# Kernel optimization log

Hardware: AMD Instinct MI355X
Metric: run time of the kernel (lower is better)

Reference implementation:

```python
import jax, jax.numpy as jnp
import numpy as np
from jax import lax

B, S, D = 4, 128, 256
POOL = 3


def conv_block(x, w, b, stride, pool_k):
    # x: (N, Cin, H, W), w: (Cout, Cin, kh, kw)
    y = lax.conv_general_dilated(
        x, w, window_strides=(stride, stride), padding='VALID',
        dimension_numbers=('NCHW', 'OIHW', 'NCHW'))
    y = y + b[None, :, None, None]
    y = jax.nn.gelu(y, approximate=False)  # torch GELU default is exact
    # MaxPool2d(kernel_size=pool_k) -> stride = pool_k, VALID
    y = lax.reduce_window(y, -jnp.inf, lax.max,
                          (1, 1, pool_k, pool_k), (1, 1, pool_k, pool_k), 'VALID')
    return y


def setup_inputs() -> dict:
    key = jax.random.key(0)
    ks = jax.random.split(key, 8)
    token_features = jax.random.normal(ks[0], (B, S, D), dtype=jnp.float32)
    type_embedds = jax.random.normal(ks[1], (B, S, D), dtype=jnp.float32)
    # Conv2dFeatures(depth=3, num_channels=16, start_kernel=3, start_stride=2, pool_kernel=3)
    w1 = jax.random.normal(ks[2], (16, 1, 3, 3), dtype=jnp.float32) * 0.1
    b1 = jax.random.normal(ks[3], (16,), dtype=jnp.float32) * 0.01
    w2 = jax.random.normal(ks[4], (32, 16, 3, 3), dtype=jnp.float32) * 0.05
    b2 = jax.random.normal(ks[5], (32,), dtype=jnp.float32) * 0.01
    w3 = jax.random.normal(ks[6], (32, 32, 3, 3), dtype=jnp.float32) * 0.05
    b3 = jax.random.normal(ks[7], (32,), dtype=jnp.float32) * 0.01
    return dict(token_features=token_features, type_embedds=type_embedds,
                w1=w1, b1=b1, w2=w2, b2=b2, w3=w3, b3=b3)


def reference(token_features, type_embedds, w1, b1, w2, b2, w3, b3):
    b, s, d = type_embedds.shape
    # Outter2dFusion: fused[n,s,i,j] = type_embedds[n,s,i] * token_features[n,s,j]
    fused = jnp.einsum('bsi,bsj->bsij', type_embedds, token_features)
    # Conv stack applied per seq position with in_channels=1 == one batched conv
    x = fused.reshape(b * s, 1, d, d)
    x = conv_block(x, w1, b1, stride=2, pool_k=POOL)
    x = conv_block(x, w2, b2, stride=1, pool_k=POOL)
    x = conv_block(x, w3, b3, stride=1, pool_k=POOL)
    # Dropout is identity in eval mode
    return x.reshape(b, s, -1)
```

## Files before the change

kernel.cpp:

```cpp
#include <hip/hip_runtime.h>
#include <math.h>


#define NIMG 512

__device__ __forceinline__ float gelu_exact(float x) {
    return 0.5f * x * (1.0f + erff(x * 0.70710678118654752f));
}
__device__ __forceinline__ float pool_gelu(float vmin, float vmax) {
    return fmaxf(gelu_exact(vmin), gelu_exact(vmax));
}

typedef __attribute__((address_space(3))) char lds_char;
typedef const __attribute__((address_space(1))) char glb_char;
__device__ __forceinline__ void gl_lds16(const void* g, void* l) {
    __builtin_amdgcn_global_load_lds((glb_char*)g, (lds_char*)l, 16, 0, 0);
}

__global__ __launch_bounds__(256) void k1_fused(const float* __restrict__ tok,
                                                const float* __restrict__ typ,
                                                const float* __restrict__ w1,
                                                const float* __restrict__ b1,
                                                float* __restrict__ s1) {
    const int blk = blockIdx.x;
    const int img = blk >> 1;
    const int py0 = (blk & 1) * 21;
    const int tid = threadIdx.x;
    const int c     = tid >> 4;
    const int pslot = tid & 15;

    float wv[9];
#pragma unroll
    for (int k = 0; k < 9; ++k) wv[k] = w1[c * 9 + k];
    const float bias = b1[c];

    const float* frow = tok + img * 256;
    const float* trow = typ + img * 256;

    float g[3][3][3];
    int pxv[3];
#pragma unroll
    for (int s = 0; s < 3; ++s) {
        const int px = pslot + 16 * s;
        pxv[s] = px;
        const int pe = px < 42 ? px : 41;
        float f7[7];
#pragma unroll
        for (int q = 0; q < 7; ++q) f7[q] = frow[6 * pe + q];
#pragma unroll
        for (int di = 0; di < 3; ++di)
#pragma unroll
            for (int wx = 0; wx < 3; ++wx)
                g[s][di][wx] = wv[di * 3 + 0] * f7[2 * wx]
                             + wv[di * 3 + 1] * f7[2 * wx + 1]
                             + wv[di * 3 + 2] * f7[2 * wx + 2];
    }

    float* orow = s1 + ((size_t)img * 16 + c) * (42 * 44);
    for (int py = py0; py < py0 + 21; ++py) {
        float ts[7];
#pragma unroll
        for (int q = 0; q < 7; ++q) ts[q] = trow[6 * py + q];
#pragma unroll
        for (int s = 0; s < 3; ++s) {
            float vmin = INFINITY, vmax = -INFINITY;
#pragma unroll
            for (int wy = 0; wy < 3; ++wy) {
#pragma unroll
                for (int wx = 0; wx < 3; ++wx) {
                    float v = ts[2 * wy] * g[s][0][wx];
                    v = fmaf(ts[2 * wy + 1], g[s][1][wx], v);
                    v = fmaf(ts[2 * wy + 2], g[s][2][wx], v);
                    vmin = fminf(vmin, v);
                    vmax = fmaxf(vmax, v);
                }
            }
            if (pxv[s] < 42)
                orow[py * 44 + pxv[s]] = pool_gelu(vmin + bias, vmax + bias);
        }
    }
}

__global__ __launch_bounds__(256) void k2_conv(const float* __restrict__ s1,
                                               const float* __restrict__ w2,
                                               const float* __restrict__ b2,
                                               float* __restrict__ s2) {
    const int blk = blockIdx.x;
    const int img = blk >> 1;
    const int cog = blk & 1;
    __shared__ float4 slab4[3][512];

    const int tid  = threadIdx.x;
    const int lane = tid & 63;
    const int grp  = tid >> 6;
    const int wbase64 = tid & ~63;

    int base[3], valid[3], py[3], px[3];
#pragma unroll
    for (int tI = 0; tI < 3; ++tI) {
        const int cc0 = lane + 64 * tI;
        valid[tI] = (cc0 < 169);
        const int cc = valid[tI] ? cc0 : 168;
        py[tI] = cc / 13;
        px[tI] = cc % 13;
        base[tI] = py[tI] * 132 + px[tI] * 3;
    }

    float acc[4][3][9];
#pragma unroll
    for (int a = 0; a < 4; ++a)
#pragma unroll
        for (int tI = 0; tI < 3; ++tI)
#pragma unroll
            for (int k = 0; k < 9; ++k) acc[a][tI][k] = 0.f;

    const float* s1img = s1 + (size_t)img * 16 * 1848;

#pragma unroll
    for (int p = 0; p < 2; ++p) {
        const char* src = (const char*)(s1img + p * 1848);
        gl_lds16(src + (size_t)tid * 16,         (char*)&slab4[p][0] + (size_t)wbase64 * 16);
        gl_lds16(src + (size_t)(256 + tid) * 16, (char*)&slab4[p][256] + (size_t)wbase64 * 16);
    }

#pragma unroll 1
    for (int cin = 0; cin < 16; ++cin) {
        const int cur = cin % 3;
        if (cin != 15) asm volatile("s_waitcnt vmcnt(2)" ::: "memory");
        else           asm volatile("s_waitcnt vmcnt(0)" ::: "memory");
        __builtin_amdgcn_s_barrier();

        if (cin + 2 < 16) {
            const int nb = (cin + 2) % 3;
            const char* src = (const char*)(s1img + (cin + 2) * 1848);
            gl_lds16(src + (size_t)tid * 16,         (char*)&slab4[nb][0] + (size_t)wbase64 * 16);
            gl_lds16(src + (size_t)(256 + tid) * 16, (char*)&slab4[nb][256] + (size_t)wbase64 * 16);
        }

        const int wb = __builtin_amdgcn_readfirstlane((cog * 16 + grp) * 144 + cin * 9);
        float wv[4][9];
#pragma unroll
        for (int a = 0; a < 4; ++a)
#pragma unroll
            for (int k = 0; k < 9; ++k) wv[a][k] = w2[wb + a * 576 + k];

        const float* slab = (const float*)&slab4[cur][0];
#pragma unroll
        for (int tI = 0; tI < 3; ++tI) {
            float win[5][5];
#pragma unroll
            for (int r = 0; r < 5; ++r)
#pragma unroll
                for (int c2 = 0; c2 < 5; ++c2)
                    win[r][c2] = slab[base[tI] + r * 44 + c2];
#pragma unroll
            for (int wy = 0; wy < 3; ++wy)
#pragma unroll
                for (int wx = 0; wx < 3; ++wx)
#pragma unroll
                    for (int dy = 0; dy < 3; ++dy)
#pragma unroll
                        for (int dx = 0; dx < 3; ++dx) {
                            const float v = win[wy + dy][wx + dx];
#pragma unroll
                            for (int a = 0; a < 4; ++a)
                                acc[a][tI][wy * 3 + wx] =
                                    fmaf(v, wv[a][dy * 3 + dx], acc[a][tI][wy * 3 + wx]);
                        }
        }
    }

#pragma unroll
    for (int tI = 0; tI < 3; ++tI) {
        if (valid[tI]) {
#pragma unroll
            for (int a = 0; a < 4; ++a) {
                float vmin = INFINITY, vmax = -INFINITY;
#pragma unroll
                for (int k = 0; k < 9; ++k) {
                    vmin = fminf(vmin, acc[a][tI][k]);
                    vmax = fmaxf(vmax, acc[a][tI][k]);
                }
                const int co = cog * 16 + grp + 4 * a;
                const float b = b2[co];
                s2[((img * 32 + co) * 13 + py[tI]) * 13 + px[tI]] =
                    pool_gelu(vmin + b, vmax + b);
            }
        }
    }
}

__global__ __launch_bounds__(192) void k3_conv(const float* __restrict__ s2,
                                               const float* __restrict__ w3,
                                               const float* __restrict__ b3,
                                               float* __restrict__ out) {
    const int img = blockIdx.x;
    __shared__ float wl[32 * 32 * 9];

    const int tid = threadIdx.x;
    for (int i = tid; i < 9216; i += 192) wl[i] = w3[i];
    __syncthreads();

    if (tid < 144) {
        const int cp   = tid / 9;
        const int cell = tid % 9;
        const int cy = cell / 3, cx = cell % 3;
        const int base = (3 * cy) * 13 + 3 * cx;
        const int co0 = 2 * cp, co1 = 2 * cp + 1;
        const float* s2img = s2 + (size_t)img * 5408 + base;

        float acc[2][9];
#pragma unroll
        for (int a = 0; a < 2; ++a)
#pragma unroll
            for (int k = 0; k < 9; ++k) acc[a][k] = 0.f;

#pragma unroll 1
        for (int cin = 0; cin < 32; ++cin) {
            const float* sl = s2img + cin * 169;
            float win[5][5];
#pragma unroll
            for (int r = 0; r < 5; ++r)
#pragma unroll
                for (int c2 = 0; c2 < 5; ++c2)
                    win[r][c2] = sl[r * 13 + c2];
            float wk[2][9];
#pragma unroll
            for (int k = 0; k < 9; ++k) {
                wk[0][k] = wl[(co0 * 32 + cin) * 9 + k];
                wk[1][k] = wl[(co1 * 32 + cin) * 9 + k];
            }
#pragma unroll
            for (int wy = 0; wy < 3; ++wy)
#pragma unroll
                for (int wx = 0; wx < 3; ++wx)
#pragma unroll
                    for (int dy = 0; dy < 3; ++dy)
#pragma unroll
                        for (int dx = 0; dx < 3; ++dx) {
                            const float v = win[wy + dy][wx + dx];
                            acc[0][wy * 3 + wx] = fmaf(v, wk[0][dy * 3 + dx], acc[0][wy * 3 + wx]);
                            acc[1][wy * 3 + wx] = fmaf(v, wk[1][dy * 3 + dx], acc[1][wy * 3 + wx]);
                        }
        }

#pragma unroll
        for (int a = 0; a < 2; ++a) {
            float vmin = INFINITY, vmax = -INFINITY;
#pragma unroll
            for (int k = 0; k < 9; ++k) {
                vmin = fminf(vmin, acc[a][k]);
                vmax = fmaxf(vmax, acc[a][k]);
            }
            const int co = a ? co1 : co0;
            const float b = b3[co];
            out[(size_t)img * 288 + co * 9 + cell] = pool_gelu(vmin + b, vmax + b);
        }
    }
}

extern "C" void kernel_launch(void* const* d_in, const int* in_sizes, int n_in,
                              void* d_out, int out_size, void* d_ws, size_t ws_size,
                              hipStream_t stream) {
    const float* tok = (const float*)d_in[0];
    const float* typ = (const float*)d_in[1];
    const float* w1  = (const float*)d_in[2];
    const float* b1  = (const float*)d_in[3];
    const float* w2  = (const float*)d_in[4];
    const float* b2  = (const float*)d_in[5];
    const float* w3  = (const float*)d_in[6];
    const float* b3  = (const float*)d_in[7];
    float* out = (float*)d_out;

    float* s1 = (float*)d_ws;
    float* s2 = s1 + (size_t)NIMG * 16 * 42 * 44;

    k1_fused<<<dim3(NIMG * 2), dim3(256), 0, stream>>>(tok, typ, w1, b1, s1);
    k2_conv<<<dim3(NIMG * 2), dim3(256), 0, stream>>>(s1, w2, b2, s2);
    k3_conv<<<dim3(NIMG), dim3(192), 0, stream>>>(s2, w3, b3, out);
}
```

Before: 254.7 us.

## Merge k2 channel-group blocks into one 512-thread block per image with bulk slab loads

k2 now uses one 512-thread block per image instead of two 256-thread blocks that each handled half the output channels. Each input slab is read from global memory once per image rather than twice. The three-slot per-channel LDS pipeline is replaced by two bulk phases, each loading 8 input channels (about 59KB of LDS) followed by a full wait. This gives up load/compute overlap and cuts occupancy, because LDS use grows and blocks get larger.

```diff
diff --git a/kernel.cpp b/kernel.cpp
--- a/kernel.cpp
+++ b/kernel.cpp
@@ -81,19 +81,16 @@
     }
 }
 
-__global__ __launch_bounds__(256) void k2_conv(const float* __restrict__ s1,
+__global__ __launch_bounds__(512) void k2_conv(const float* __restrict__ s1,
                                                const float* __restrict__ w2,
                                                const float* __restrict__ b2,
                                                float* __restrict__ s2) {
-    const int blk = blockIdx.x;
-    const int img = blk >> 1;
-    const int cog = blk & 1;
-    __shared__ float4 slab4[3][512];
+    const int img = blockIdx.x;
+    __shared__ float slab[8 * 1848];
 
     const int tid  = threadIdx.x;
     const int lane = tid & 63;
     const int grp  = tid >> 6;
-    const int wbase64 = tid & ~63;
 
     int base[3], valid[3], py[3], px[3];
 #pragma unroll
@@ -116,57 +113,50 @@
 
     const float* s1img = s1 + (size_t)img * 16 * 1848;
 
-#pragma unroll
+#pragma unroll 1
     for (int p = 0; p < 2; ++p) {
-        const char* src = (const char*)(s1img + p * 1848);
-        gl_lds16(src + (size_t)tid * 16,         (char*)&slab4[p][0] + (size_t)wbase64 * 16);
-        gl_lds16(src + (size_t)(256 + tid) * 16, (char*)&slab4[p][256] + (size_t)wbase64 * 16);
-    }
-
-#pragma unroll 1
-    for (int cin = 0; cin < 16; ++cin) {
-        const int cur = cin % 3;
-        if (cin != 15) asm volatile("s_waitcnt vmcnt(2)" ::: "memory");
-        else           asm volatile("s_waitcnt vmcnt(0)" ::: "memory");
-        __builtin_amdgcn_s_barrier();
-
-        if (cin + 2 < 16) {
-            const int nb = (cin + 2) % 3;
-            const char* src = (const char*)(s1img + (cin + 2) * 1848);
-            gl_lds16(src + (size_t)tid * 16,         (char*)&slab4[nb][0] + (size_t)wbase64 * 16);
-            gl_lds16(src + (size_t)(256 + tid) * 16, (char*)&slab4[nb][256] + (size_t)wbase64 * 16);
-        }
-
-        const int wb = __builtin_amdgcn_readfirstlane((cog * 16 + grp) * 144 + cin * 9);
-        float wv[4][9];
-#pragma unroll
-        for (int a = 0; a < 4; ++a)
-#pragma unroll
-            for (int k = 0; k < 9; ++k) wv[a][k] = w2[wb + a * 576 + k];
-
-        const float* slab = (const float*)&slab4[cur][0];
-#pragma unroll
-        for (int tI = 0; tI < 3; ++tI) {
-            float win[5][5];
-#pragma unroll
-            for (int r = 0; r < 5; ++r)
-#pragma unroll
-                for (int c2 = 0; c2 < 5; ++c2)
-                    win[r][c2] = slab[base[tI] + r * 44 + c2];
-#pragma unroll
-            for (int wy = 0; wy < 3; ++wy)
-#pragma unroll
-                for (int wx = 0; wx < 3; ++wx)
-#pragma unroll
-                    for (int dy = 0; dy < 3; ++dy)
-#pragma unroll
-                        for (int dx = 0; dx < 3; ++dx) {
-                            const float v = win[wy + dy][wx + dx];
-#pragma unroll
-                            for (int a = 0; a < 4; ++a)
-                                acc[a][tI][wy * 3 + wx] =
-                                    fmaf(v, wv[a][dy * 3 + dx], acc[a][tI][wy * 3 + wx]);
-                        }
+        __syncthreads();
+        const char* src = (const char*)(s1img + p * (8 * 1848));
+#pragma unroll 1
+        for (int i = tid; i < 3696; i += 512)
+            gl_lds16(src + (size_t)i * 16, (char*)slab + (size_t)(i & ~63) * 16);
+        asm volatile("s_waitcnt vmcnt(0)" ::: "memory");
+        __syncthreads();
+
+#pragma unroll 1
+        for (int c8 = 0; c8 < 8; ++c8) {
+            const int cin = p * 8 + c8;
+            const int wb = __builtin_amdgcn_readfirstlane((grp * 16 + cin) * 9);
+            float wv[4][9];
+#pragma unroll
+            for (int a = 0; a < 4; ++a)
+#pragma unroll
+                for (int k = 0; k < 9; ++k) wv[a][k] = w2[wb + a * 1152 + k];
+
+            const float* slabc = slab + c8 * 1848;
+#pragma unroll
+            for (int tI = 0; tI < 3; ++tI) {
+                float win[5][5];
+#pragma unroll
+                for (int r = 0; r < 5; ++r)
+#pragma unroll
+                    for (int c2 = 0; c2 < 5; ++c2)
+                        win[r][c2] = slabc[base[tI] + r * 44 + c2];
+#pragma unroll
+                for (int wy = 0; wy < 3; ++wy)
+#pragma unroll
+                    for (int wx = 0; wx < 3; ++wx)
+#pragma unroll
+                        for (int dy = 0; dy < 3; ++dy)
+#pragma unroll
+                            for (int dx = 0; dx < 3; ++dx) {
+                                const float v = win[wy + dy][wx + dx];
+#pragma unroll
+                                for (int a = 0; a < 4; ++a)
+                                    acc[a][tI][wy * 3 + wx] =
+                                        fmaf(v, wv[a][dy * 3 + dx], acc[a][tI][wy * 3 + wx]);
+                            }
+            }
         }
     }
 
@@ -181,7 +171,7 @@
                     vmin = fminf(vmin, acc[a][tI][k]);
                     vmax = fmaxf(vmax, acc[a][tI][k]);
                 }
-                const int co = cog * 16 + grp + 4 * a;
+                const int co = grp + 8 * a;
                 const float b = b2[co];
                 s2[((img * 32 + co) * 13 + py[tI]) * 13 + px[tI]] =
                     pool_gelu(vmin + b, vmax + b);
@@ -276,6 +266,6 @@
     float* s2 = s1 + (size_t)NIMG * 16 * 42 * 44;
 
     k1_fused<<<dim3(NIMG * 2), dim3(256), 0, stream>>>(tok, typ, w1, b1, s1);
-    k2_conv<<<dim3(NIMG * 2), dim3(256), 0, stream>>>(s1, w2, b2, s2);
+    k2_conv<<<dim3(NIMG), dim3(512), 0, stream>>>(s1, w2, b2, s2);
     k3_conv<<<dim3(NIMG), dim3(192), 0, stream>>>(s2, w3, b3, out);
 }
```

Result: no change. 258.1 us (+1.3%).
